# Kernel optimization log

Measured on AMD Instinct MI355X. Metric: run time of the kernel, lower is better.

Reference implementation:

```python
import jax, jax.numpy as jnp
import numpy as np

B, S, D_MODEL, HEADS = 2, 2048, 1024, 16
K_D = D_MODEL // HEADS


def setup_inputs() -> dict:
    key = jax.random.key(0)
    ks = jax.random.split(key, 5)
    x = jax.random.normal(ks[0], (B, S, D_MODEL), dtype=jnp.float32)
    # causal mask, 1 = keep, 0 = masked (GPT-2 style)
    mask = jnp.tril(jnp.ones((S, S), dtype=jnp.int32))[None, None, :, :]
    sc = 0.02
    w_attn = jax.random.normal(ks[1], (D_MODEL, 3 * D_MODEL), dtype=jnp.float32) * sc
    b_attn = jax.random.normal(ks[2], (3 * D_MODEL,), dtype=jnp.float32) * sc
    w_proj = jax.random.normal(ks[3], (D_MODEL, D_MODEL), dtype=jnp.float32) * sc
    b_proj = jax.random.normal(ks[4], (D_MODEL,), dtype=jnp.float32) * sc
    return {"x": x, "mask": mask, "w_attn": w_attn, "b_attn": b_attn,
            "w_proj": w_proj, "b_proj": b_proj}


def reference(x, mask, w_attn, b_attn, w_proj, b_proj):
    b, s, _ = x.shape
    qkv = x @ w_attn + b_attn                      # [B,S,3*d_model]
    # NOTE: source assigns value, query, key = split(...) in that order
    v, q, k = jnp.split(qkv, 3, axis=-1)
    def heads(t):  # [B,S,d_model] -> [B,H,S,k_d]
        return t.reshape(b, s, HEADS, K_D).transpose(0, 2, 1, 3)
    v, q, k = heads(v), heads(q), heads(k)
    present = jnp.stack((k, v))                    # [2,B,H,S,k_d]
    scores = jnp.einsum('bhqd,bhkd->bhqk', q, k) / jnp.sqrt(jnp.float32(K_D))
    scores = jnp.where(mask == 0, -jnp.inf, scores)
    attn = jax.nn.softmax(scores, axis=-1)         # [B,H,S,S]
    out = jnp.einsum('bhqk,bhkd->bhqd', attn, v)   # [B,H,S,k_d]
    out = out.transpose(0, 2, 1, 3).reshape(b, s, D_MODEL)
    out = out @ w_proj + b_proj
    return out, present
```

## Files before the change

kernel.cpp:

```cpp
#include <hip/hip_runtime.h>
#include <math.h>

constexpr int BB = 2;
constexpr int SS = 2048;
constexpr int DM = 1024;
constexpr int NH = 16;
constexpr int KD = 64;
constexpr int OUT_ELEMS  = BB*SS*DM;
constexpr int PRES_HALF  = BB*NH*SS*KD;
#define NEGSENT (-1e30f)

typedef __attribute__((ext_vector_type(8))) short short8;
typedef __attribute__((ext_vector_type(4))) short short4v;
typedef __attribute__((ext_vector_type(4))) float f32x4;

__device__ __forceinline__ float us2f(unsigned short u) {
  union { unsigned int ui; float f; } c; c.ui = ((unsigned int)u) << 16; return c.f;
}
__device__ __forceinline__ short f2s(float f) {
  union { float f; unsigned int u; } c; c.f = f;
  return (short)((c.u + 0x7FFFu + ((c.u >> 16) & 1u)) >> 16);
}
__device__ __forceinline__ short f2s_hw(float f) {
  unsigned int r;
  asm("v_cvt_pk_bf16_f32 %0, %1, %1" : "=v"(r) : "v"(f));
  return (short)r;
}
__device__ __forceinline__ unsigned int pk2(float lo, float hi) {
  unsigned int r;
  asm("v_cvt_pk_bf16_f32 %0, %1, %2" : "=v"(r) : "v"(lo), "v"(hi));
  return r;
}

#define GLOAD_LDS16(g, l) \
  __builtin_amdgcn_global_load_lds((const __attribute__((address_space(1))) void*)(g), \
                                   (__attribute__((address_space(3))) void*)(l), 16, 0, 0)

__global__ __launch_bounds__(256)
void prep_k(const float* __restrict__ x, short* __restrict__ xb,
            const float* __restrict__ wa, short* __restrict__ wat,
            const float* __restrict__ wp, short* __restrict__ wpt) {
  __shared__ float tl[32][33];
  const int bid = blockIdx.x;
  if (bid < 4096) {
    const size_t i = ((size_t)bid * 256 + threadIdx.x) * 4;
    const float4 v = *(const float4*)(x + i);
    uint2 o; o.x = pk2(v.x, v.y); o.y = pk2(v.z, v.w);
    *(uint2*)(xb + i) = o;
    return;
  }
  const float* w; short* wt; int N, t;
  if (bid < 4096 + 3072) { w = wa; wt = wat; N = 3 * DM; t = bid - 4096; }
  else { w = wp; wt = wpt; N = DM; t = bid - 7168; }
  const int nb = (N == DM) ? 32 : 96;
  const int n0 = (t % nb) * 32, k0 = (t / nb) * 32;
  const int tx = threadIdx.x & 31, ty = threadIdx.x >> 5;
  #pragma unroll
  for (int i = 0; i < 4; ++i) {
    const int kk = ty + i * 8;
    tl[kk][tx] = w[(size_t)(k0 + kk) * N + n0 + tx];
  }
  __syncthreads();
  #pragma unroll
  for (int i = 0; i < 4; ++i) {
    const int nn = ty + i * 8;
    wt[(size_t)(n0 + nn) * 1024 + k0 + tx] = f2s(tl[tx][nn]);
  }
}

__global__ __launch_bounds__(256)
void v_tr_k(const float* __restrict__ vf, short* __restrict__ vt) {
  __shared__ float tl[64][65];
  const int bh = blockIdx.x;
  const int s0 = blockIdx.y * 64;
  const int tr = threadIdx.x >> 2;
  const int tc = (threadIdx.x & 3) * 16;
  const float* src = vf + ((size_t)bh * SS + s0) * KD;
  #pragma unroll
  for (int i = 0; i < 4; ++i) {
    const float4 v = *(const float4*)(src + (size_t)tr * KD + tc + i * 4);
    tl[tr][tc + i * 4 + 0] = v.x; tl[tr][tc + i * 4 + 1] = v.y;
    tl[tr][tc + i * 4 + 2] = v.z; tl[tr][tc + i * 4 + 3] = v.w;
  }
  __syncthreads();
  uint4 o0, o1;
  unsigned int* p0 = (unsigned int*)&o0;
  unsigned int* p1 = (unsigned int*)&o1;
  #pragma unroll
  for (int j = 0; j < 4; ++j) {
    int pos = tc + 2 * j;
    int k0 = (pos & 32) | ((pos & 31) >> 1) | ((pos & 1) << 4);
    int k1 = ((pos + 1) & 32) | (((pos + 1) & 31) >> 1) | (((pos + 1) & 1) << 4);
    p0[j] = pk2(tl[k0][tr], tl[k1][tr]);
  }
  #pragma unroll
  for (int j = 0; j < 4; ++j) {
    int pos = tc + 8 + 2 * j;
    int k0 = (pos & 32) | ((pos & 31) >> 1) | ((pos & 1) << 4);
    int k1 = ((pos + 1) & 32) | (((pos + 1) & 31) >> 1) | (((pos + 1) & 1) << 4);
    p1[j] = pk2(tl[k0][tr], tl[k1][tr]);
  }
  short* dst = vt + ((size_t)bh * KD + tr) * SS + s0 + tc;
  *(uint4*)(dst) = o0;
  *(uint4*)(dst + 8) = o1;
}

__device__ __forceinline__ void mfma_tile_loop(
    const short* __restrict__ A, const short* __restrict__ Bt,
    int m0, int n0, short* Asm, short* Bsm, f32x4 (*acc)[4]) {
  const int tid = threadIdx.x;
  const int lane = tid & 63;
  const int w = tid >> 6;
  const int wm = (w >> 1) * 64, wn = (w & 1) * 64;
  const int ln15 = lane & 15, quad = lane >> 4;
  for (int k0 = 0; k0 < 1024; k0 += 32) {
    #pragma unroll
    for (int j = 0; j < 2; ++j) {
      const int e = j * 256 + tid;
      const int r = e >> 2, cq = e & 3;
      GLOAD_LDS16(A  + (size_t)(m0 + r) * 1024 + k0 + cq * 8, Asm + e * 8);
      GLOAD_LDS16(Bt + (size_t)(n0 + r) * 1024 + k0 + cq * 8, Bsm + e * 8);
    }
    __syncthreads();
    short8 af[4], bf[4];
    #pragma unroll
    for (int t = 0; t < 4; ++t)
      af[t] = *(const short8*)(Asm + (wm + t * 16 + ln15) * 32 + quad * 8);
    #pragma unroll
    for (int t = 0; t < 4; ++t)
      bf[t] = *(const short8*)(Bsm + (wn + t * 16 + ln15) * 32 + quad * 8);
    #pragma unroll
    for (int tm = 0; tm < 4; ++tm)
      #pragma unroll
      for (int tn = 0; tn < 4; ++tn)
        acc[tm][tn] = __builtin_amdgcn_mfma_f32_16x16x32_bf16(
            af[tm], bf[tn], acc[tm][tn], 0, 0, 0);
    __syncthreads();
  }
}

__global__ __launch_bounds__(256)
void qkv_mfma_k(const short* __restrict__ A, const short* __restrict__ Bt,
                const float* __restrict__ bias, short* __restrict__ qbf,
                float* __restrict__ outf, short* __restrict__ kbf) {
  __shared__ short Asm[128 * 32];
  __shared__ short Bsm[128 * 32];
  const int n0 = blockIdx.x * 128, m0 = blockIdx.y * 128;
  f32x4 acc[4][4] = {};
  mfma_tile_loop(A, Bt, m0, n0, Asm, Bsm, acc);
  const int lane = threadIdx.x & 63;
  const int w = threadIdx.x >> 6;
  const int wm = (w >> 1) * 64, wn = (w & 1) * 64;
  const int col = lane & 15, row4 = (lane >> 4) * 4;
  const int mbase = m0 + wm;
  const int bb = mbase >> 11;
  const int sbase = (mbase & 2047) + row4;
  #pragma unroll
  for (int tn = 0; tn < 4; ++tn) {
    const int n = n0 + wn + tn * 16 + col;
    const float bv = bias[n];
    const int c = n & 1023, h = c >> 6, d = c & 63;
    const size_t base = ((size_t)(bb * NH + h) * SS) * KD + d;
    #pragma unroll
    for (int tm = 0; tm < 4; ++tm) {
      const size_t sb = base + (size_t)(sbase + tm * 16) * KD;
      #pragma unroll
      for (int r = 0; r < 4; ++r) {
        const float val = acc[tm][tn][r] + bv;
        const size_t idx = sb + (size_t)r * KD;
        if (n < DM) {
          outf[(size_t)OUT_ELEMS + (size_t)PRES_HALF + idx] = val;
        } else if (n < 2 * DM) {
          qbf[idx] = f2s_hw(val);
        } else {
          outf[(size_t)OUT_ELEMS + idx] = val;
          if (kbf) kbf[idx] = f2s_hw(val);
        }
      }
    }
  }
}

__global__ __launch_bounds__(256)
void proj_mfma_k(const short* __restrict__ A, const short* __restrict__ Bt,
                 const float* __restrict__ bias, float* __restrict__ outf) {
  __shared__ short Asm[128 * 32];
  __shared__ short Bsm[64 * 32];
  const int n0 = blockIdx.x * 64, m0 = blockIdx.y * 128;
  const int tid = threadIdx.x;
  const int lane = tid & 63;
  const int w = tid >> 6;
  const int wm = (w >> 1) * 64, wn = (w & 1) * 32;
  const int ln15 = lane & 15, quad = lane >> 4;
  f32x4 acc[4][2] = {};
  for (int k0 = 0; k0 < 1024; k0 += 32) {
    #pragma unroll
    for (int j = 0; j < 2; ++j) {
      const int e = j * 256 + tid;
      const int r = e >> 2, cq = e & 3;
      GLOAD_LDS16(A + (size_t)(m0 + r) * 1024 + k0 + cq * 8, Asm + e * 8);
    }
    {
      const int r = tid >> 2, cq = tid & 3;
      GLOAD_LDS16(Bt + (size_t)(n0 + r) * 1024 + k0 + cq * 8, Bsm + tid * 8);
    }
    __syncthreads();
    short8 af[4], bf[2];
    #pragma unroll
    for (int t = 0; t < 4; ++t)
      af[t] = *(const short8*)(Asm + (wm + t * 16 + ln15) * 32 + quad * 8);
    #pragma unroll
    for (int t = 0; t < 2; ++t)
      bf[t] = *(const short8*)(Bsm + (wn + t * 16 + ln15) * 32 + quad * 8);
    #pragma unroll
    for (int tm = 0; tm < 4; ++tm)
      #pragma unroll
      for (int tn = 0; tn < 2; ++tn)
        acc[tm][tn] = __builtin_amdgcn_mfma_f32_16x16x32_bf16(
            af[tm], bf[tn], acc[tm][tn], 0, 0, 0);
    __syncthreads();
  }
  const int col = ln15, row4 = quad * 4;
  #pragma unroll
  for (int tm = 0; tm < 4; ++tm) {
    #pragma unroll
    for (int tn = 0; tn < 2; ++tn) {
      const int n = n0 + wn + tn * 16 + col;
      const float b = bias[n];
      #pragma unroll
      for (int r = 0; r < 4; ++r) {
        const int m = m0 + wm + tm * 16 + row4 + r;
        outf[(size_t)m * DM + n] = acc[tm][tn][r] + b;
      }
    }
  }
}

__device__ __forceinline__ void stage_kv4(const short* __restrict__ Kg,
                                          const short* __restrict__ Vg,
                                          int kb, short* Ksb, short* Vtb,
                                          int tid) {
  #pragma unroll
  for (int rd = 0; rd < 2; ++rd) {
    const int i = rd * 256 + tid;
    const int row = i >> 3, grp = i & 7;
    const int sw = (grp ^ (row & 7)) << 3;
    GLOAD_LDS16(Kg + (size_t)(kb + row) * KD + sw, Ksb + i * 8);
    GLOAD_LDS16(Vg + (size_t)row * SS + kb + sw, Vtb + i * 8);
  }
}

__global__ __launch_bounds__(256)
void attn_mfma9_k(const short* __restrict__ qbf, const short* __restrict__ kbf,
                  const short* __restrict__ vbft, short* __restrict__ obf) {
  __shared__ short Ks[2][64 * 64];
  __shared__ short Vt[2][64 * 64];
  __shared__ short Ps[4][16 * 64];
  const int bid = blockIdx.x;
  const int xcd = bid & 7, g = bid >> 3;
  const int rnd = g >> 4;
  const int p   = g & 15;
  const int bh  = (xcd << 2) | rnd;
  const int tid = threadIdx.x;
  const int w   = tid >> 6;
  const int lane = tid & 63;
  const int ln15 = lane & 15, quad = lane >> 4;
  const int rswz = (ln15 & 7) << 3;
  const float SC2 = 0.125f * 1.44269504f;
  const float THR = 8.0f;

  const short* Kg = kbf  + (size_t)bh * SS * KD;
  const short* Vg = vbft + (size_t)bh * KD * SS;
  short* Pw = Ps[w];
  const int bb = bh >> 4, h = bh & 15;

  #pragma unroll 1
  for (int pass = 0; pass < 2; ++pass) {
    const int qb = pass ? (31 - p) : p;
    const int q0 = qb * 64;
    const int nch = qb + 1;

    short8 aq[2];
    {
      const short* qp = qbf + ((size_t)bh * SS + q0 + w * 16) * KD;
      aq[0] = *(const short8*)(qp + (size_t)ln15 * KD + quad * 8);
      aq[1] = *(const short8*)(qp + (size_t)ln15 * KD + 32 + quad * 8);
    }
    f32x4 O[4] = {};
    float mreg[4], lreg[4];
    #pragma unroll
    for (int r = 0; r < 4; ++r) { mreg[r] = NEGSENT; lreg[r] = 0.f; }

    stage_kv4(Kg, Vg, 0, Ks[0], Vt[0], tid);
    __syncthreads();

    for (int ch = 0; ch < nch; ++ch) {
      const int cur = ch & 1;
      if (ch + 1 < nch)
        stage_kv4(Kg, Vg, (ch + 1) * 64, Ks[cur ^ 1], Vt[cur ^ 1], tid);
      const short* Kc = Ks[cur];
      const short* Vc = Vt[cur];

      f32x4 S[4] = {};
      #pragma unroll
      for (int kt = 0; kt < 2; ++kt) {
        short8 bk[4];
        #pragma unroll
        for (int tn = 0; tn < 4; ++tn)
          bk[tn] = *(const short8*)(Kc + (tn * 16 + ln15) * 64 + ((kt * 32 + quad * 8) ^ rswz));
        #pragma unroll
        for (int tn = 0; tn < 4; ++tn)
          S[tn] = __builtin_amdgcn_mfma_f32_16x16x32_bf16(aq[kt], bk[tn], S[tn], 0, 0, 0);
      }

      if (ch == qb) {
        const int rowl = w * 16 + quad * 4;
        #pragma unroll
        for (int tn = 0; tn < 4; ++tn) {
          const int colk = tn * 16 + ln15;
          #pragma unroll
          for (int r = 0; r < 4; ++r)
            if (colk > rowl + r) S[tn][r] = NEGSENT;
        }
      }

      {
        float lmax = S[0][0];
        #pragma unroll
        for (int tn = 0; tn < 4; ++tn)
          #pragma unroll
          for (int r = 0; r < 4; ++r) lmax = fmaxf(lmax, S[tn][r]);
        const float mmin = fminf(fminf(mreg[0], mreg[1]), fminf(mreg[2], mreg[3]));
        const bool ok = (lmax - mmin) <= THR;
        if (!__all((int)ok)) {
          #pragma unroll
          for (int r = 0; r < 4; ++r) {
            float mx = fmaxf(fmaxf(fmaxf(S[0][r], S[1][r]), S[2][r]), S[3][r]);
            mx = fmaxf(mx, __shfl_xor(mx, 1, 64));
            mx = fmaxf(mx, __shfl_xor(mx, 2, 64));
            mx = fmaxf(mx, __shfl_xor(mx, 4, 64));
            mx = fmaxf(mx, __shfl_xor(mx, 8, 64));
            const float mn = fmaxf(mreg[r], mx);
            const float al = exp2f((mreg[r] - mn) * SC2);
            mreg[r] = mn;
            lreg[r] *= al;
            O[0][r] *= al; O[1][r] *= al; O[2][r] *= al; O[3][r] *= al;
          }
        }
      }

      #pragma unroll
      for (int r = 0; r < 4; ++r) {
        const float mnsc = mreg[r] * SC2;
        const int prow = quad * 4 + r;
        const int rs = (prow & 7) << 3;
        float p0 = exp2f(fmaf(S[0][r], SC2, -mnsc));
        float p1 = exp2f(fmaf(S[1][r], SC2, -mnsc));
        float p2 = exp2f(fmaf(S[2][r], SC2, -mnsc));
        float p3 = exp2f(fmaf(S[3][r], SC2, -mnsc));
        lreg[r] += (p0 + p1) + (p2 + p3);
        *(unsigned int*)(Pw + prow * 64 + ((2 * ln15) ^ rs))      = pk2(p0, p1);
        *(unsigned int*)(Pw + prow * 64 + ((32 + 2 * ln15) ^ rs)) = pk2(p2, p3);
      }
      asm volatile("s_waitcnt lgkmcnt(0)" ::: "memory");
      __builtin_amdgcn_sched_barrier(0);

      #pragma unroll
      for (int kt = 0; kt < 2; ++kt) {
        short8 ap = *(const short8*)(Pw + ln15 * 64 + ((kt * 32 + quad * 8) ^ rswz));
        short8 bv[4];
        #pragma unroll
        for (int tn = 0; tn < 4; ++tn)
          bv[tn] = *(const short8*)(Vc + (tn * 16 + ln15) * 64 + ((kt * 32 + quad * 8) ^ rswz));
        #pragma unroll
        for (int tn = 0; tn < 4; ++tn)
          O[tn] = __builtin_amdgcn_mfma_f32_16x16x32_bf16(ap, bv[tn], O[tn], 0, 0, 0);
      }
      __syncthreads();
    }

    #pragma unroll
    for (int r = 0; r < 4; ++r) {
      float l = lreg[r];
      l += __shfl_xor(l, 1, 64);
      l += __shfl_xor(l, 2, 64);
      l += __shfl_xor(l, 4, 64);
      l += __shfl_xor(l, 8, 64);
      lreg[r] = 1.f / fmaxf(l, 1e-30f);
    }
    short* ob = obf + ((size_t)bb * SS + q0 + w * 16) * DM + h * KD;
    #pragma unroll
    for (int tn = 0; tn < 4; ++tn)
      #pragma unroll
      for (int r = 0; r < 4; ++r)
        ob[(size_t)(quad * 4 + r) * DM + tn * 16 + ln15] = f2s_hw(O[tn][r] * lreg[r]);
  }
}

__global__ __launch_bounds__(256)
void attn_k(const short* __restrict__ qbf, const float* __restrict__ pres,
            short* __restrict__ obf) {
  __shared__ float Ksf[32][64];
  __shared__ float Vsf[32][64];
  const int bh = blockIdx.x;
  const int q0 = ((int)gridDim.y - 1 - (int)blockIdx.y) * 64;
  const int t  = threadIdx.x;
  const int part = t & 3;
  const int row  = t >> 2;
  const int qr   = q0 + row;
  const int dbase = part * 16;
  const size_t qoff = ((size_t)bh * SS + qr) * KD + dbase;
  float q[16], o[16];
  #pragma unroll
  for (int i = 0; i < 16; ++i) q[i] = us2f((unsigned short)qbf[qoff + i]);
  #pragma unroll
  for (int i = 0; i < 16; ++i) o[i] = 0.f;
  float m = NEGSENT, l = 0.f;
  const float* Kb = pres + (size_t)bh * SS * KD;
  const float* Vb = pres + (size_t)PRES_HALF + (size_t)bh * SS * KD;
  const int nch = (q0 + 64) / 32;
  for (int ch = 0; ch < nch; ++ch) {
    const int kbase = ch * 32;
    __syncthreads();
    {
      const float4* ksrc = (const float4*)(Kb + (size_t)kbase * KD);
      const float4* vsrc = (const float4*)(Vb + (size_t)kbase * KD);
      float4* kdst = (float4*)&Ksf[0][0];
      float4* vdst = (float4*)&Vsf[0][0];
      #pragma unroll
      for (int i = 0; i < 2; ++i) {
        kdst[t + i * 256] = ksrc[t + i * 256];
        vdst[t + i * 256] = vsrc[t + i * 256];
      }
    }
    __syncthreads();
    float sc[32];
    #pragma unroll
    for (int kk = 0; kk < 32; ++kk) {
      float s = 0.f;
      #pragma unroll
      for (int i = 0; i < 16; ++i) s = fmaf(q[i], Ksf[kk][dbase + i], s);
      s += __shfl_xor(s, 1, 64);
      s += __shfl_xor(s, 2, 64);
      sc[kk] = (kbase + kk <= qr) ? s * 0.125f : NEGSENT;
    }
    float mc = sc[0];
    #pragma unroll
    for (int kk = 1; kk < 32; ++kk) mc = fmaxf(mc, sc[kk]);
    const float mn = fmaxf(m, mc);
    const float alpha = __expf(m - mn);
    l *= alpha;
    #pragma unroll
    for (int i = 0; i < 16; ++i) o[i] *= alpha;
    #pragma unroll
    for (int kk = 0; kk < 32; ++kk) {
      const float p = __expf(sc[kk] - mn);
      l += p;
      #pragma unroll
      for (int i = 0; i < 16; ++i) o[i] = fmaf(p, Vsf[kk][dbase + i], o[i]);
    }
    m = mn;
  }
  const float inv = 1.f / fmaxf(l, 1e-30f);
  const int bb = bh >> 4, h = bh & 15;
  const size_t ooff = ((size_t)(bb * SS + qr)) * DM + h * KD + dbase;
  #pragma unroll
  for (int i = 0; i < 16; ++i) obf[ooff + i] = f2s(o[i] * inv);
}

extern "C" void kernel_launch(void* const* d_in, const int* in_sizes, int n_in,
                              void* d_out, int out_size, void* d_ws, size_t ws_size,
                              hipStream_t stream) {
  const float* x      = (const float*)d_in[0];
  const float* w_attn = (const float*)d_in[2];
  const float* b_attn = (const float*)d_in[3];
  const float* w_proj = (const float*)d_in[4];
  const float* b_proj = (const float*)d_in[5];
  float* outf = (float*)d_out;

  constexpr size_t MB = 1024 * 1024;
  if (ws_size >= 24 * MB) {
    short* ws0   = (short*)d_ws;
    short* x_bf  = ws0;
    short* o_bf  = ws0;
    short* wat_t = ws0 + (size_t)4 * 1024 * 1024;
    short* wpt_t = ws0 + (size_t)7 * 1024 * 1024;
    short* q_bf  = ws0 + (size_t)8 * 1024 * 1024;
    short* k_bf  = (short*)d_out;
    short* v_bft = k_bf + (size_t)PRES_HALF;

    prep_k<<<8192, 256, 0, stream>>>(x, x_bf, w_attn, wat_t, w_proj, wpt_t);

    qkv_mfma_k<<<dim3(24, 32), 256, 0, stream>>>(x_bf, wat_t, b_attn, q_bf, outf,
                                                 k_bf);

    v_tr_k<<<dim3(BB * NH, SS / 64), 256, 0, stream>>>(
        outf + OUT_ELEMS + PRES_HALF, v_bft);

    attn_mfma9_k<<<dim3(512), 256, 0, stream>>>(q_bf, k_bf, v_bft, o_bf);

    proj_mfma_k<<<dim3(16, 32), 256, 0, stream>>>(o_bf, wpt_t, b_proj, outf);
  } else {
    short* x_bf;
    short* q_bf;
    short* wat_t;
    short* wpt_t;
    short* o_bf;
    if (ws_size >= 16 * MB) {
      short* ws = (short*)d_ws;
      x_bf  = (short*)d_out;
      q_bf  = x_bf + OUT_ELEMS;
      wat_t = ws;
      wpt_t = wat_t + 3 * DM * DM;
      o_bf  = wat_t + 4 * DM * DM;
    } else {
      x_bf  = (short*)d_out;
      q_bf  = x_bf + OUT_ELEMS;
      wat_t = (short*)d_in[1];
      wpt_t = wat_t + 3 * DM * DM;
      o_bf  = wat_t + 4 * DM * DM;
    }
    prep_k<<<8192, 256, 0, stream>>>(x, x_bf, w_attn, wat_t, w_proj, wpt_t);
    qkv_mfma_k<<<dim3(24, 32), 256, 0, stream>>>(x_bf, wat_t, b_attn, q_bf, outf,
                                                 nullptr);
    attn_k<<<dim3(BB * NH, SS / 64), 256, 0, stream>>>(q_bf, outf + OUT_ELEMS, o_bf);
    proj_mfma_k<<<dim3(16, 32), 256, 0, stream>>>(o_bf, wpt_t, b_proj, outf);
  }
}
```

Measured before the change: 219.3 us.

## Double-buffer LDS tiles in QKV/proj GEMMs and remap blocks per XCD

The QKV and projection MFMA GEMMs now use two LDS buffers. The next k-slice's global-to-LDS loads are issued before the current slice's MFMAs run, which removes one barrier per iteration and overlaps load latency with compute. The launch grids are also flattened to 1D, and block indices are remapped so that blocks landing on the same XCD share A rows and B columns, to improve L2 reuse. This doubles the LDS use per block, which could reduce occupancy.

```diff
diff --git a/kernel.cpp b/kernel.cpp
--- a/kernel.cpp
+++ b/kernel.cpp
@@ -105,6 +105,18 @@
   *(uint4*)(dst + 8) = o1;
 }
 
+__device__ __forceinline__ void stage_ab(const short* __restrict__ A,
+                                         const short* __restrict__ Bt,
+                                         int m0, int n0, int k0,
+                                         short* Asb, short* Bsb, int tid) {
+  #pragma unroll
+  for (int j = 0; j < 2; ++j) {
+    const int e = j * 256 + tid;
+    const int r = e >> 2, cq = e & 3;
+    GLOAD_LDS16(A  + (size_t)(m0 + r) * 1024 + k0 + cq * 8, Asb + e * 8);
+    GLOAD_LDS16(Bt + (size_t)(n0 + r) * 1024 + k0 + cq * 8, Bsb + e * 8);
+  }
+}
 __device__ __forceinline__ void mfma_tile_loop(
     const short* __restrict__ A, const short* __restrict__ Bt,
     int m0, int n0, short* Asm, short* Bsm, f32x4 (*acc)[4]) {
@@ -113,22 +125,22 @@
   const int w = tid >> 6;
   const int wm = (w >> 1) * 64, wn = (w & 1) * 64;
   const int ln15 = lane & 15, quad = lane >> 4;
+  stage_ab(A, Bt, m0, n0, 0, Asm, Bsm, tid);
+  __syncthreads();
   for (int k0 = 0; k0 < 1024; k0 += 32) {
-    #pragma unroll
-    for (int j = 0; j < 2; ++j) {
-      const int e = j * 256 + tid;
-      const int r = e >> 2, cq = e & 3;
-      GLOAD_LDS16(A  + (size_t)(m0 + r) * 1024 + k0 + cq * 8, Asm + e * 8);
-      GLOAD_LDS16(Bt + (size_t)(n0 + r) * 1024 + k0 + cq * 8, Bsm + e * 8);
-    }
-    __syncthreads();
+    const int cur = (k0 >> 5) & 1;
+    if (k0 + 32 < 1024)
+      stage_ab(A, Bt, m0, n0, k0 + 32,
+               Asm + (cur ^ 1) * (128 * 32), Bsm + (cur ^ 1) * (128 * 32), tid);
+    const short* Ac = Asm + cur * (128 * 32);
+    const short* Bc = Bsm + cur * (128 * 32);
     short8 af[4], bf[4];
     #pragma unroll
     for (int t = 0; t < 4; ++t)
-      af[t] = *(const short8*)(Asm + (wm + t * 16 + ln15) * 32 + quad * 8);
+      af[t] = *(const short8*)(Ac + (wm + t * 16 + ln15) * 32 + quad * 8);
     #pragma unroll
     for (int t = 0; t < 4; ++t)
-      bf[t] = *(const short8*)(Bsm + (wn + t * 16 + ln15) * 32 + quad * 8);
+      bf[t] = *(const short8*)(Bc + (wn + t * 16 + ln15) * 32 + quad * 8);
     #pragma unroll
     for (int tm = 0; tm < 4; ++tm)
       #pragma unroll
@@ -143,11 +155,15 @@
 void qkv_mfma_k(const short* __restrict__ A, const short* __restrict__ Bt,
                 const float* __restrict__ bias, short* __restrict__ qbf,
                 float* __restrict__ outf, short* __restrict__ kbf) {
-  __shared__ short Asm[128 * 32];
-  __shared__ short Bsm[128 * 32];
-  const int n0 = blockIdx.x * 128, m0 = blockIdx.y * 128;
+  __shared__ short Asm[2][128 * 32];
+  __shared__ short Bsm[2][128 * 32];
+  const int bid = blockIdx.x;
+  const int xcd = bid & 7, g = bid >> 3;
+  const int mp = ((xcd >> 1) << 3) | (g & 7);
+  const int np = (xcd & 1) * 12 + (g >> 3);
+  const int n0 = np * 128, m0 = mp * 128;
   f32x4 acc[4][4] = {};
-  mfma_tile_loop(A, Bt, m0, n0, Asm, Bsm, acc);
+  mfma_tile_loop(A, Bt, m0, n0, &Asm[0][0], &Bsm[0][0], acc);
   const int lane = threadIdx.x & 63;
   const int w = threadIdx.x >> 6;
   const int wm = (w >> 1) * 64, wn = (w & 1) * 64;
@@ -184,34 +200,52 @@
 __global__ __launch_bounds__(256)
 void proj_mfma_k(const short* __restrict__ A, const short* __restrict__ Bt,
                  const float* __restrict__ bias, float* __restrict__ outf) {
-  __shared__ short Asm[128 * 32];
-  __shared__ short Bsm[64 * 32];
-  const int n0 = blockIdx.x * 64, m0 = blockIdx.y * 128;
+  __shared__ short Asm[2][128 * 32];
+  __shared__ short Bsm[2][64 * 32];
+  const int bid = blockIdx.x;
+  const int xcd = bid & 7, g = bid >> 3;
+  const int m0 = ((xcd << 2) | (g & 3)) * 128;
+  const int n0 = (g >> 2) * 64;
   const int tid = threadIdx.x;
   const int lane = tid & 63;
   const int w = tid >> 6;
   const int wm = (w >> 1) * 64, wn = (w & 1) * 32;
   const int ln15 = lane & 15, quad = lane >> 4;
   f32x4 acc[4][2] = {};
-  for (int k0 = 0; k0 < 1024; k0 += 32) {
+  {
     #pragma unroll
     for (int j = 0; j < 2; ++j) {
       const int e = j * 256 + tid;
       const int r = e >> 2, cq = e & 3;
-      GLOAD_LDS16(A + (size_t)(m0 + r) * 1024 + k0 + cq * 8, Asm + e * 8);
-    }
-    {
+      GLOAD_LDS16(A + (size_t)(m0 + r) * 1024 + cq * 8, &Asm[0][0] + e * 8);
+    }
+    const int r = tid >> 2, cq = tid & 3;
+    GLOAD_LDS16(Bt + (size_t)(n0 + r) * 1024 + cq * 8, &Bsm[0][0] + tid * 8);
+  }
+  __syncthreads();
+  for (int k0 = 0; k0 < 1024; k0 += 32) {
+    const int cur = (k0 >> 5) & 1;
+    if (k0 + 32 < 1024) {
+      short* Asb = &Asm[cur ^ 1][0];
+      short* Bsb = &Bsm[cur ^ 1][0];
+      #pragma unroll
+      for (int j = 0; j < 2; ++j) {
+        const int e = j * 256 + tid;
+        const int r = e >> 2, cq = e & 3;
+        GLOAD_LDS16(A + (size_t)(m0 + r) * 1024 + k0 + 32 + cq * 8, Asb + e * 8);
+      }
       const int r = tid >> 2, cq = tid & 3;
-      GLOAD_LDS16(Bt + (size_t)(n0 + r) * 1024 + k0 + cq * 8, Bsm + tid * 8);
-    }
-    __syncthreads();
+      GLOAD_LDS16(Bt + (size_t)(n0 + r) * 1024 + k0 + 32 + cq * 8, Bsb + tid * 8);
+    }
+    const short* Ac = &Asm[cur][0];
+    const short* Bc = &Bsm[cur][0];
     short8 af[4], bf[2];
     #pragma unroll
     for (int t = 0; t < 4; ++t)
-      af[t] = *(const short8*)(Asm + (wm + t * 16 + ln15) * 32 + quad * 8);
+      af[t] = *(const short8*)(Ac + (wm + t * 16 + ln15) * 32 + quad * 8);
     #pragma unroll
     for (int t = 0; t < 2; ++t)
-      bf[t] = *(const short8*)(Bsm + (wn + t * 16 + ln15) * 32 + quad * 8);
+      bf[t] = *(const short8*)(Bc + (wn + t * 16 + ln15) * 32 + quad * 8);
     #pragma unroll
     for (int tm = 0; tm < 4; ++tm)
       #pragma unroll
@@ -491,15 +525,14 @@
 
     prep_k<<<8192, 256, 0, stream>>>(x, x_bf, w_attn, wat_t, w_proj, wpt_t);
 
-    qkv_mfma_k<<<dim3(24, 32), 256, 0, stream>>>(x_bf, wat_t, b_attn, q_bf, outf,
-                                                 k_bf);
+    qkv_mfma_k<<<768, 256, 0, stream>>>(x_bf, wat_t, b_attn, q_bf, outf, k_bf);
 
     v_tr_k<<<dim3(BB * NH, SS / 64), 256, 0, stream>>>(
         outf + OUT_ELEMS + PRES_HALF, v_bft);
 
     attn_mfma9_k<<<dim3(512), 256, 0, stream>>>(q_bf, k_bf, v_bft, o_bf);
 
-    proj_mfma_k<<<dim3(16, 32), 256, 0, stream>>>(o_bf, wpt_t, b_proj, outf);
+    proj_mfma_k<<<512, 256, 0, stream>>>(o_bf, wpt_t, b_proj, outf);
   } else {
     short* x_bf;
     short* q_bf;
@@ -521,9 +554,8 @@
       o_bf  = wat_t + 4 * DM * DM;
     }
     prep_k<<<8192, 256, 0, stream>>>(x, x_bf, w_attn, wat_t, w_proj, wpt_t);
-    qkv_mfma_k<<<dim3(24, 32), 256, 0, stream>>>(x_bf, wat_t, b_attn, q_bf, outf,
-                                                 nullptr);
+    qkv_mfma_k<<<768, 256, 0, stream>>>(x_bf, wat_t, b_attn, q_bf, outf, nullptr);
     attn_k<<<dim3(BB * NH, SS / 64), 256, 0, stream>>>(q_bf, outf + OUT_ELEMS, o_bf);
-    proj_mfma_k<<<dim3(16, 32), 256, 0, stream>>>(o_bf, wpt_t, b_proj, outf);
-  }
-}
+    proj_mfma_k<<<512, 256, 0, stream>>>(o_bf, wpt_t, b_proj, outf);
+  }
+}
```

After: 225.5 us. +2.8%, slower.
